# Performance work log

Measured on AMD Instinct MI355X. Metric: run time of the kernel, lower is better.

## Reference

```python
import jax, jax.numpy as jnp
import numpy as np

B, H, T, NCLS = 4096, 300, 43, 80


def setup_inputs() -> dict:
    key = jax.random.key(0)
    ks = jax.random.split(key, 8)
    s = 0.05  # weight init scale
    return {
        "x": jax.random.normal(ks[0], (B, H, T), dtype=jnp.float32),
        "w_ih": jax.random.normal(ks[1], (2, 4 * H, H), dtype=jnp.float32) * s,
        "w_hh": jax.random.normal(ks[2], (2, 4 * H, H), dtype=jnp.float32) * s,
        "b_ih": jax.random.normal(ks[3], (2, 4 * H), dtype=jnp.float32) * s,
        "b_hh": jax.random.normal(ks[4], (2, 4 * H), dtype=jnp.float32) * s,
        "conv_w": jax.random.normal(ks[5], (H,), dtype=jnp.float32) * s,
        "fc_w": jax.random.normal(ks[6], (NCLS, H), dtype=jnp.float32) * s,
        "fc_b": jax.random.normal(ks[7], (NCLS,), dtype=jnp.float32) * s,
    }


def reference(x, w_ih, w_hh, b_ih, b_hh, conv_w, fc_w, fc_b):
    # x: [B, 300, 43]. Each step feeds x[:, :, t] (seq_len=1 LSTM call) to BOTH
    # directions of the 'bidirectional' LSTM, carrying states forward in time.
    # => two independent forward LSTMs (d=0,1) whose hidden states are summed.
    batch = x.shape[0]
    xs = jnp.transpose(x, (2, 0, 1))  # [T, B, H]
    bias = (b_ih + b_hh)[:, None, :]  # [2, 1, 4H]

    def step(carry, xt):
        h, c = carry  # each [2, B, H]
        z = (jnp.einsum('bi,dgi->dbg', xt, w_ih)
             + jnp.einsum('dbh,dgh->dbg', h, w_hh) + bias)  # [2, B, 4H]
        i, f, g, o = jnp.split(z, 4, axis=-1)  # torch gate order i,f,g,o
        c_new = jax.nn.sigmoid(f) * c + jax.nn.sigmoid(i) * jnp.tanh(g)
        h_new = jax.nn.sigmoid(o) * jnp.tanh(c_new)
        return (h_new, c_new), h_new.sum(0)  # sum over the 2 directions

    h0 = jnp.zeros((2, batch, x.shape[1]), dtype=x.dtype)
    _, hsum = jax.lax.scan(step, (h0, h0), xs)  # hsum: [T, B, H]

    hStates = jnp.transpose(hsum, (1, 2, 0))          # [B, H, T]
    M = jnp.tanh(hStates)
    alpha = jnp.einsum('bht,h->bt', M, conv_w)        # conv1d(H->1, k=1), no bias
    alpha = jax.nn.softmax(alpha, axis=-1)            # softmax over time
    r = jnp.einsum('bht,bt->bh', hStates, alpha)      # bmm(hStates, alpha)
    hStar = jnp.tanh(r)                               # [B, H]
    out = hStar @ fc_w.T + fc_b                       # [B, 80]
    return jax.nn.softmax(out, axis=1)
```

## Files before the change

kernel.cpp:

```cpp
#include <hip/hip_runtime.h>
#include <cstdint>
#include <cstddef>

#define B_  4096
#define H_  300
#define T_  43
#define NC_ 80
#define HP  320
#define ND  1280
#define NDD 2560
#define TR  304
#define SB2 (T_ * TR)
#define XZC 4

typedef _Float16 f16;
typedef _Float16 half8 __attribute__((ext_vector_type(8)));
typedef _Float16 half4 __attribute__((ext_vector_type(4)));
typedef float    f32x4 __attribute__((ext_vector_type(4)));

__device__ __forceinline__ void gl_lds16(const void* g, void* l) {
  __builtin_amdgcn_global_load_lds(
      (const __attribute__((address_space(1))) void*)g,
      (__attribute__((address_space(3))) void*)l, 16, 0, 0);
}
__device__ __forceinline__ float sigmoid_(float x) {
  return 1.f / (1.f + __expf(-x));
}
__device__ __forceinline__ float tanh_fast(float x) {
  x = fminf(fmaxf(x, -15.f), 15.f);
  float e = __expf(2.f * x);
  return (e - 1.f) / (e + 1.f);
}

__global__ void prep_weights(const float* __restrict__ w_ih,
                             const float* __restrict__ w_hh,
                             const float* __restrict__ b_ih,
                             const float* __restrict__ b_hh,
                             f16* __restrict__ Wih, f16* __restrict__ Whh,
                             float* __restrict__ bias) {
  int idx = blockIdx.x * 256 + threadIdx.x;
  const int total = NDD * HP;
  if (idx < 2 * total) {
    int which = idx / total;
    int rem = idx % total;
    int row = rem / HP, k = rem % HP;
    int d = row / ND, n = row % ND;
    int jh = n >> 2, g = n & 3;
    float v = 0.f;
    if (jh < H_ && k < H_) {
      const float* W = which ? w_hh : w_ih;
      v = W[((size_t)d * 4 * H_ + g * H_ + jh) * H_ + k];
    }
    (which ? Whh : Wih)[(size_t)row * HP + k] = (f16)v;
  }
  if (idx < NDD) {
    int d = idx / ND, n = idx % ND;
    int jh = n >> 2, g = n & 3;
    float v = 0.f;
    if (jh < H_)
      v = b_ih[d * 4 * H_ + g * H_ + jh] + b_hh[d * 4 * H_ + g * H_ + jh];
    bias[idx] = v;
  }
}

__global__ void prep_xT(const float* __restrict__ x, f16* __restrict__ xT) {
  __shared__ float tile[64][44];
  int b = blockIdx.x, ch = blockIdx.y;
  int h0 = ch * 64;
  for (int idx = threadIdx.x; idx < 64 * T_; idx += 256) {
    int hh = idx / T_, t = idx % T_;
    float v = 0.f;
    if (h0 + hh < H_) v = x[((size_t)b * H_ + h0 + hh) * T_ + t];
    tile[hh][t] = v;
  }
  __syncthreads();
  for (int idx = threadIdx.x; idx < 64 * T_; idx += 256) {
    int t = idx / 64, hh = idx % 64;
    xT[((size_t)t * B_ + b) * HP + h0 + hh] = (f16)tile[hh][t];
  }
}

__global__ void xz_gemm(const f16* __restrict__ Xc,
                        const f16* __restrict__ Wih,
                        half4* __restrict__ xz4) {
  __shared__ f16 As[128 * 32];
  __shared__ f16 Bs[128 * 32];
  const int tid = threadIdx.x;
  const int wave = tid >> 6, lane = tid & 63;
  const int mt = blockIdx.x, nt = blockIdx.y;
  const int lrow4 = lane >> 2, col8 = (lane & 3) << 3;
  const int wm = wave & 1, wn = wave >> 1;
  const int lr = lane & 15, lq = lane >> 4;
  const int kq = lq << 3;

  const f16* Ab = Wih + (size_t)nt * 128 * HP;
  const f16* Bb = Xc + (size_t)mt * 128 * HP;

  f32x4 acc[4][4];
#pragma unroll
  for (int i = 0; i < 4; i++)
#pragma unroll
    for (int j = 0; j < 4; j++) acc[i][j] = (f32x4){0.f, 0.f, 0.f, 0.f};

  for (int kt = 0; kt < HP / 32; ++kt) {
    __syncthreads();
#pragma unroll
    for (int i = 0; i < 2; i++) {
      int r0 = wave * 32 + i * 16;
      gl_lds16(Ab + (size_t)(r0 + lrow4) * HP + kt * 32 + col8, &As[r0 * 32]);
      gl_lds16(Bb + (size_t)(r0 + lrow4) * HP + kt * 32 + col8, &Bs[r0 * 32]);
    }
    __syncthreads();
    half8 af[4], bf[4];
#pragma unroll
    for (int i = 0; i < 4; i++) {
      af[i] = *(const half8*)&As[(wm * 64 + i * 16 + lr) * 32 + kq];
      bf[i] = *(const half8*)&Bs[(wn * 64 + i * 16 + lr) * 32 + kq];
    }
#pragma unroll
    for (int i = 0; i < 4; i++)
#pragma unroll
      for (int j = 0; j < 4; j++)
        acc[i][j] = __builtin_amdgcn_mfma_f32_16x16x32_f16(af[i], bf[j],
                                                           acc[i][j], 0, 0, 0);
  }

  const int dt = nt / 10;
  const int tl = mt >> 5;
#pragma unroll
  for (int i = 0; i < 4; i++) {
    const int jh = (nt % 10) * 32 + wm * 16 + i * 4 + lq;
    if (jh >= H_) continue;
#pragma unroll
    for (int j = 0; j < 4; j++) {
      const int b = (mt & 31) * 128 + wn * 64 + j * 16 + lr;
      half4 o;
#pragma unroll
      for (int r = 0; r < 4; r++) o[r] = (f16)acc[i][j][r];
      xz4[((size_t)(tl * 2 + dt) * HP + jh) * B_ + b] = o;
    }
  }
}

__global__ void lstm_step(const f16* __restrict__ h_prev,
                          f16* __restrict__ h_next,
                          float* __restrict__ c,
                          const f16* __restrict__ Whh,
                          const float* __restrict__ bias,
                          const half4* __restrict__ xz4,
                          f16* __restrict__ hs,
                          int t)
{
  __shared__ __attribute__((aligned(16))) char smem[16384];
  f16* As = (f16*)smem;
  f16* Bs = (f16*)(smem + 8192);
  f16* tile = (f16*)smem;

  const int tid = threadIdx.x;
  const int wave = tid >> 6, lane = tid & 63;
  const int wt = blockIdx.x, bt = blockIdx.y, d = blockIdx.z;
  const int lrow4 = lane >> 2, col8 = (lane & 3) << 3;
  const int wm = wave & 1, wn = wave >> 1;
  const int lr = lane & 15, lq = lane >> 4;
  const int kq = lq << 3;

  const f16* Wb = Whh + ((size_t)d * ND + wt * 128) * HP;
  const f16* hb = h_prev + ((size_t)d * B_ + bt * 128) * HP;

  f32x4 acc[4][4];
#pragma unroll
  for (int i = 0; i < 4; i++)
#pragma unroll
    for (int j = 0; j < 4; j++) acc[i][j] = (f32x4){0.f, 0.f, 0.f, 0.f};

  for (int kt = 0; kt < HP / 32; ++kt) {
    __syncthreads();
#pragma unroll
    for (int i = 0; i < 2; i++) {
      int r0 = wave * 32 + i * 16;
      gl_lds16(Wb + (size_t)(r0 + lrow4) * HP + kt * 32 + col8, &As[r0 * 32]);
      gl_lds16(hb + (size_t)(r0 + lrow4) * HP + kt * 32 + col8, &Bs[r0 * 32]);
    }
    __syncthreads();
    half8 af[4], bf[4];
#pragma unroll
    for (int i = 0; i < 4; i++) {
      af[i] = *(const half8*)&As[(wm * 64 + i * 16 + lr) * 32 + kq];
      bf[i] = *(const half8*)&Bs[(wn * 64 + i * 16 + lr) * 32 + kq];
    }
#pragma unroll
    for (int i = 0; i < 4; i++)
#pragma unroll
      for (int j = 0; j < 4; j++)
        acc[i][j] = __builtin_amdgcn_mfma_f32_16x16x32_f16(af[i], bf[j],
                                                           acc[i][j], 0, 0, 0);
  }

  __syncthreads();

#pragma unroll
  for (int i = 0; i < 4; i++) {
    const int jl = wm * 16 + i * 4 + lq;
    const int jh = wt * 32 + jl;
    float4 b4 = {0.f, 0.f, 0.f, 0.f};
    if (jh < H_) b4 = *(const float4*)&bias[d * ND + 4 * jh];
#pragma unroll
    for (int j = 0; j < 4; j++) {
      const int bl = wn * 64 + j * 16 + lr;
      const int b = bt * 128 + bl;
      f16 hnv = (f16)0.f;
      if (jh < H_) {
        const half4 x4 = xz4[((size_t)d * HP + jh) * B_ + b];
        float zi = acc[i][j][0] + b4.x + (float)x4[0];
        float zf = acc[i][j][1] + b4.y + (float)x4[1];
        float zg = acc[i][j][2] + b4.z + (float)x4[2];
        float zo = acc[i][j][3] + b4.w + (float)x4[3];
        const size_t cidx = ((size_t)d * H_ + jh) * B_ + b;
        float co = c[cidx];
        float cn = sigmoid_(zf) * co + sigmoid_(zi) * tanh_fast(zg);
        float hn = sigmoid_(zo) * tanh_fast(cn);
        c[cidx] = cn;
        hnv = (f16)hn;
      }
      tile[jl * 136 + bl] = hnv;
    }
  }
  __syncthreads();

  {
    const int bl = tid >> 1, jhalf = tid & 1;
    const int b = bt * 128 + bl;
    f16 vals[16];
#pragma unroll
    for (int jj = 0; jj < 16; jj++)
      vals[jj] = tile[(jhalf * 16 + jj) * 136 + bl];
    half8 v0, v1;
#pragma unroll
    for (int r = 0; r < 8; r++) { v0[r] = vals[r]; v1[r] = vals[8 + r]; }

    const int jh0 = wt * 32 + jhalf * 16;
    f16* hdst = h_next + ((size_t)d * B_ + b) * HP + jh0;
    *(half8*)hdst = v0;
    *(half8*)(hdst + 8) = v1;

    if (jh0 < H_) {
      f16* sdst = hs + ((size_t)d * B_ + b) * SB2 + t * TR + jh0;
      *(half8*)sdst = v0;
      *(half8*)(sdst + 8) = v1;
    }
  }
}

__global__ __launch_bounds__(256) void attn1(const f16* __restrict__ hs,
                                             const float* __restrict__ conv_w,
                                             float* __restrict__ alpha_g) {
  __shared__ float cw[TR];
  __shared__ float red[48];
  const int b = blockIdx.x, tid = threadIdx.x;
  const int wave = tid >> 6, lane = tid & 63;
  for (int k = tid; k < TR; k += 256) cw[k] = (k < H_) ? conv_w[k] : 0.f;
  __syncthreads();

  const half4* s0 = (const half4*)(hs + (size_t)b * SB2);
  const half4* s1 = (const half4*)(hs + (size_t)(B_ + b) * SB2);
  for (int t = wave; t < T_; t += 4) {
    const int base = t * (TR / 4);
    float p = 0.f;
    {
      half4 a = s0[base + lane], cc = s1[base + lane];
#pragma unroll
      for (int r = 0; r < 4; r++)
        p += tanh_fast((float)a[r] + (float)cc[r]) * cw[lane * 4 + r];
    }
    if (lane < 12) {
      half4 a = s0[base + 64 + lane], cc = s1[base + 64 + lane];
#pragma unroll
      for (int r = 0; r < 4; r++)
        p += tanh_fast((float)a[r] + (float)cc[r]) * cw[256 + lane * 4 + r];
    }
#pragma unroll
    for (int o = 32; o; o >>= 1) p += __shfl_down(p, o);
    if (lane == 0) red[t] = p;
  }
  __syncthreads();
  if (tid < 64) {
    float a = (tid < T_) ? red[tid] : -1e30f;
    float mx = a;
#pragma unroll
    for (int o = 32; o; o >>= 1) mx = fmaxf(mx, __shfl_xor(mx, o));
    float e = (tid < T_) ? __expf(a - mx) : 0.f;
    float s = e;
#pragma unroll
    for (int o = 32; o; o >>= 1) s += __shfl_xor(s, o);
    if (tid < T_) alpha_g[(size_t)b * 44 + tid] = e / s;
  }
}

__global__ __launch_bounds__(256) void attn2(const f16* __restrict__ hs,
                                             const float* __restrict__ alpha_g,
                                             const float* __restrict__ fc_w,
                                             const float* __restrict__ fc_b,
                                             float* __restrict__ out) {
  __shared__ float al[T_];
  __shared__ float hstar[TR];
  __shared__ float lg[NC_];
  const int b = blockIdx.x, tid = threadIdx.x;
  if (tid < T_) al[tid] = alpha_g[(size_t)b * 44 + tid];
  __syncthreads();

  const f16* s0 = hs + (size_t)b * SB2;
  const f16* s1 = hs + (size_t)(B_ + b) * SB2;
  float r0 = 0.f, r1 = 0.f;
  for (int t = 0; t < T_; t++) {
    const float a = al[t];
    r0 += ((float)s0[t * TR + tid] + (float)s1[t * TR + tid]) * a;
    if (tid < 48)
      r1 += ((float)s0[t * TR + 256 + tid] + (float)s1[t * TR + 256 + tid]) * a;
  }
  hstar[tid] = tanh_fast(r0);
  if (tid < 48) hstar[256 + tid] = tanh_fast(r1);
  __syncthreads();

  const int wave = tid >> 6, lane = tid & 63;
  for (int cls = wave; cls < NC_; cls += 4) {
    float p = 0.f;
    for (int k = lane; k < H_; k += 64) p += hstar[k] * fc_w[(size_t)cls * H_ + k];
#pragma unroll
    for (int o = 32; o; o >>= 1) p += __shfl_down(p, o);
    if (lane == 0) lg[cls] = p + fc_b[cls];
  }
  __syncthreads();
  if (tid < 64) {
    float a0 = (tid < 40) ? lg[tid] : -1e30f;
    float a1 = (tid < 40) ? lg[tid + 40] : -1e30f;
    float mx = fmaxf(a0, a1);
#pragma unroll
    for (int o = 32; o; o >>= 1) mx = fmaxf(mx, __shfl_xor(mx, o));
    float e0 = (tid < 40) ? __expf(a0 - mx) : 0.f;
    float e1 = (tid < 40) ? __expf(a1 - mx) : 0.f;
    float s = e0 + e1;
#pragma unroll
    for (int o = 32; o; o >>= 1) s += __shfl_xor(s, o);
    if (tid < 40) {
      out[(size_t)b * NC_ + tid] = e0 / s;
      out[(size_t)b * NC_ + tid + 40] = e1 / s;
    }
  }
}

extern "C" void kernel_launch(void* const* d_in, const int* in_sizes, int n_in,
                              void* d_out, int out_size, void* d_ws, size_t ws_size,
                              hipStream_t stream) {
  const float* x      = (const float*)d_in[0];
  const float* w_ih   = (const float*)d_in[1];
  const float* w_hh   = (const float*)d_in[2];
  const float* b_ih   = (const float*)d_in[3];
  const float* b_hh   = (const float*)d_in[4];
  const float* conv_w = (const float*)d_in[5];
  const float* fc_w   = (const float*)d_in[6];
  const float* fc_b   = (const float*)d_in[7];
  float* out = (float*)d_out;

  char* p = (char*)d_ws;
  f16* Wih = (f16*)p;   p += (size_t)NDD * HP * sizeof(f16);
  f16* Whh = (f16*)p;   p += (size_t)NDD * HP * sizeof(f16);
  float* bias = (float*)p; p += (size_t)NDD * sizeof(float);
  p = (char*)(((uintptr_t)p + 255) & ~(uintptr_t)255);
  f16* xT = (f16*)p;    p += (size_t)T_ * B_ * HP * sizeof(f16);
  f16* h  = (f16*)p;    p += (size_t)2 * 2 * B_ * HP * sizeof(f16);
  float* c = (float*)p; p += (size_t)2 * B_ * H_ * sizeof(float);
  f16* hs = (f16*)p;    p += (size_t)2 * B_ * SB2 * sizeof(f16);
  half4* xz = (half4*)p; p += (size_t)XZC * 2 * HP * B_ * sizeof(half4);
  float* alpha_g = (float*)p; p += (size_t)B_ * 44 * sizeof(float);

  hipMemsetAsync(h, 0, (size_t)2 * 2 * B_ * HP * sizeof(f16), stream);
  hipMemsetAsync(c, 0, (size_t)2 * B_ * H_ * sizeof(float), stream);

  prep_weights<<<(2 * NDD * HP + 255) / 256, 256, 0, stream>>>(
      w_ih, w_hh, b_ih, b_hh, Wih, Whh, bias);
  prep_xT<<<dim3(B_, 5), 256, 0, stream>>>(x, xT);

  const size_t hstride = (size_t)2 * B_ * HP;
  const size_t xzslab = (size_t)2 * HP * B_;
  int t0 = 0;
  while (t0 < T_) {
    int cn = (T_ - t0 < XZC) ? (T_ - t0) : XZC;
    xz_gemm<<<dim3(cn * 32, 20), 256, 0, stream>>>(
        xT + (size_t)t0 * B_ * HP, Wih, xz);
    for (int tt = 0; tt < cn; ++tt) {
      int t = t0 + tt;
      lstm_step<<<dim3(10, 32, 2), 256, 0, stream>>>(
          h + (size_t)(t & 1) * hstride, h + (size_t)((t + 1) & 1) * hstride,
          c, Whh, bias, xz + (size_t)tt * xzslab, hs, t);
    }
    t0 += cn;
  }

  attn1<<<B_, 256, 0, stream>>>(hs, conv_w, alpha_g);
  attn2<<<B_, 256, 0, stream>>>(hs, alpha_g, fc_w, fc_b, out);
}
```

Before: 2.069 ms.

## Double-buffer LDS tiles in GEMMs and read recurrent h directly from hs

Both xz_gemm and lstm_step now use two LDS buffers, so the next K-slice is loaded while MFMAs run on the current one, with one barrier per iteration instead of two. The h ping-pong buffers are removed: each step reads the previous hidden state straight out of the hs history with a strided layout, and a zeroed buffer stands in for t=0. This drops one global store per step and the extra h buffer. The cost is twice the LDS per block, which can lower occupancy. There is also a risk: the 320-wide K loop now reads past the 304-wide hs slot into the next timestep's slot, which is never initialised. Those values are multiplied by zero-padded weights, but NaN or Inf garbage there could still corrupt the result.

```diff
diff --git a/kernel.cpp b/kernel.cpp
--- a/kernel.cpp
+++ b/kernel.cpp
@@ -83,8 +83,8 @@
 __global__ void xz_gemm(const f16* __restrict__ Xc,
                         const f16* __restrict__ Wih,
                         half4* __restrict__ xz4) {
-  __shared__ f16 As[128 * 32];
-  __shared__ f16 Bs[128 * 32];
+  __shared__ __attribute__((aligned(16))) f16 As[2][4096];
+  __shared__ __attribute__((aligned(16))) f16 Bs[2][4096];
   const int tid = threadIdx.x;
   const int wave = tid >> 6, lane = tid & 63;
   const int mt = blockIdx.x, nt = blockIdx.y;
@@ -102,20 +102,30 @@
 #pragma unroll
     for (int j = 0; j < 4; j++) acc[i][j] = (f32x4){0.f, 0.f, 0.f, 0.f};
 
+#pragma unroll
+  for (int i2 = 0; i2 < 2; i2++) {
+    int r0 = wave * 32 + i2 * 16;
+    gl_lds16(Ab + (size_t)(r0 + lrow4) * HP + col8, &As[0][r0 * 32]);
+    gl_lds16(Bb + (size_t)(r0 + lrow4) * HP + col8, &Bs[0][r0 * 32]);
+  }
+  __syncthreads();
+
   for (int kt = 0; kt < HP / 32; ++kt) {
-    __syncthreads();
-#pragma unroll
-    for (int i = 0; i < 2; i++) {
-      int r0 = wave * 32 + i * 16;
-      gl_lds16(Ab + (size_t)(r0 + lrow4) * HP + kt * 32 + col8, &As[r0 * 32]);
-      gl_lds16(Bb + (size_t)(r0 + lrow4) * HP + kt * 32 + col8, &Bs[r0 * 32]);
-    }
-    __syncthreads();
+    const int cur = kt & 1;
+    if (kt + 1 < HP / 32) {
+      const int nk = (kt + 1) * 32;
+#pragma unroll
+      for (int i2 = 0; i2 < 2; i2++) {
+        int r0 = wave * 32 + i2 * 16;
+        gl_lds16(Ab + (size_t)(r0 + lrow4) * HP + nk + col8, &As[cur ^ 1][r0 * 32]);
+        gl_lds16(Bb + (size_t)(r0 + lrow4) * HP + nk + col8, &Bs[cur ^ 1][r0 * 32]);
+      }
+    }
     half8 af[4], bf[4];
 #pragma unroll
     for (int i = 0; i < 4; i++) {
-      af[i] = *(const half8*)&As[(wm * 64 + i * 16 + lr) * 32 + kq];
-      bf[i] = *(const half8*)&Bs[(wn * 64 + i * 16 + lr) * 32 + kq];
+      af[i] = *(const half8*)&As[cur][(wm * 64 + i * 16 + lr) * 32 + kq];
+      bf[i] = *(const half8*)&Bs[cur][(wn * 64 + i * 16 + lr) * 32 + kq];
     }
 #pragma unroll
     for (int i = 0; i < 4; i++)
@@ -123,6 +133,7 @@
       for (int j = 0; j < 4; j++)
         acc[i][j] = __builtin_amdgcn_mfma_f32_16x16x32_f16(af[i], bf[j],
                                                            acc[i][j], 0, 0, 0);
+    __syncthreads();
   }
 
   const int dt = nt / 10;
@@ -142,8 +153,8 @@
   }
 }
 
-__global__ void lstm_step(const f16* __restrict__ h_prev,
-                          f16* __restrict__ h_next,
+__global__ void lstm_step(const f16* __restrict__ hprev,
+                          long bstride, long dstride,
                           float* __restrict__ c,
                           const f16* __restrict__ Whh,
                           const float* __restrict__ bias,
@@ -151,10 +162,9 @@
                           f16* __restrict__ hs,
                           int t)
 {
-  __shared__ __attribute__((aligned(16))) char smem[16384];
-  f16* As = (f16*)smem;
-  f16* Bs = (f16*)(smem + 8192);
-  f16* tile = (f16*)smem;
+  __shared__ __attribute__((aligned(16))) f16 As[2][4096];
+  __shared__ __attribute__((aligned(16))) f16 Bs[2][4096];
+  f16* tile = &As[0][0];
 
   const int tid = threadIdx.x;
   const int wave = tid >> 6, lane = tid & 63;
@@ -165,7 +175,7 @@
   const int kq = lq << 3;
 
   const f16* Wb = Whh + ((size_t)d * ND + wt * 128) * HP;
-  const f16* hb = h_prev + ((size_t)d * B_ + bt * 128) * HP;
+  const f16* hb = hprev + (size_t)d * dstride + (size_t)(bt * 128) * bstride;
 
   f32x4 acc[4][4];
 #pragma unroll
@@ -173,30 +183,40 @@
 #pragma unroll
     for (int j = 0; j < 4; j++) acc[i][j] = (f32x4){0.f, 0.f, 0.f, 0.f};
 
+#pragma unroll
+  for (int i2 = 0; i2 < 2; i2++) {
+    int r0 = wave * 32 + i2 * 16;
+    gl_lds16(Wb + (size_t)(r0 + lrow4) * HP + col8, &As[0][r0 * 32]);
+    gl_lds16(hb + (size_t)(r0 + lrow4) * bstride + col8, &Bs[0][r0 * 32]);
+  }
+  __syncthreads();
+
   for (int kt = 0; kt < HP / 32; ++kt) {
+    const int cur = kt & 1;
+    if (kt + 1 < HP / 32) {
+      const int nk = (kt + 1) * 32;
+#pragma unroll
+      for (int i2 = 0; i2 < 2; i2++) {
+        int r0 = wave * 32 + i2 * 16;
+        gl_lds16(Wb + (size_t)(r0 + lrow4) * HP + nk + col8, &As[cur ^ 1][r0 * 32]);
+        gl_lds16(hb + (size_t)(r0 + lrow4) * bstride + nk + col8,
+                 &Bs[cur ^ 1][r0 * 32]);
+      }
+    }
+    half8 af[4], bf8[4];
+#pragma unroll
+    for (int i = 0; i < 4; i++) {
+      af[i] = *(const half8*)&As[cur][(wm * 64 + i * 16 + lr) * 32 + kq];
+      bf8[i] = *(const half8*)&Bs[cur][(wn * 64 + i * 16 + lr) * 32 + kq];
+    }
+#pragma unroll
+    for (int i = 0; i < 4; i++)
+#pragma unroll
+      for (int j = 0; j < 4; j++)
+        acc[i][j] = __builtin_amdgcn_mfma_f32_16x16x32_f16(af[i], bf8[j],
+                                                           acc[i][j], 0, 0, 0);
     __syncthreads();
-#pragma unroll
-    for (int i = 0; i < 2; i++) {
-      int r0 = wave * 32 + i * 16;
-      gl_lds16(Wb + (size_t)(r0 + lrow4) * HP + kt * 32 + col8, &As[r0 * 32]);
-      gl_lds16(hb + (size_t)(r0 + lrow4) * HP + kt * 32 + col8, &Bs[r0 * 32]);
-    }
-    __syncthreads();
-    half8 af[4], bf[4];
-#pragma unroll
-    for (int i = 0; i < 4; i++) {
-      af[i] = *(const half8*)&As[(wm * 64 + i * 16 + lr) * 32 + kq];
-      bf[i] = *(const half8*)&Bs[(wn * 64 + i * 16 + lr) * 32 + kq];
-    }
-#pragma unroll
-    for (int i = 0; i < 4; i++)
-#pragma unroll
-      for (int j = 0; j < 4; j++)
-        acc[i][j] = __builtin_amdgcn_mfma_f32_16x16x32_f16(af[i], bf[j],
-                                                           acc[i][j], 0, 0, 0);
-  }
-
-  __syncthreads();
+  }
 
 #pragma unroll
   for (int i = 0; i < 4; i++) {
@@ -230,20 +250,15 @@
   {
     const int bl = tid >> 1, jhalf = tid & 1;
     const int b = bt * 128 + bl;
-    f16 vals[16];
-#pragma unroll
-    for (int jj = 0; jj < 16; jj++)
-      vals[jj] = tile[(jhalf * 16 + jj) * 136 + bl];
-    half8 v0, v1;
-#pragma unroll
-    for (int r = 0; r < 8; r++) { v0[r] = vals[r]; v1[r] = vals[8 + r]; }
-
     const int jh0 = wt * 32 + jhalf * 16;
-    f16* hdst = h_next + ((size_t)d * B_ + b) * HP + jh0;
-    *(half8*)hdst = v0;
-    *(half8*)(hdst + 8) = v1;
-
     if (jh0 < H_) {
+      f16 vals[16];
+#pragma unroll
+      for (int jj = 0; jj < 16; jj++)
+        vals[jj] = tile[(jhalf * 16 + jj) * 136 + bl];
+      half8 v0, v1;
+#pragma unroll
+      for (int r = 0; r < 8; r++) { v0[r] = vals[r]; v1[r] = vals[8 + r]; }
       f16* sdst = hs + ((size_t)d * B_ + b) * SB2 + t * TR + jh0;
       *(half8*)sdst = v0;
       *(half8*)(sdst + 8) = v1;
@@ -367,20 +382,19 @@
   float* bias = (float*)p; p += (size_t)NDD * sizeof(float);
   p = (char*)(((uintptr_t)p + 255) & ~(uintptr_t)255);
   f16* xT = (f16*)p;    p += (size_t)T_ * B_ * HP * sizeof(f16);
-  f16* h  = (f16*)p;    p += (size_t)2 * 2 * B_ * HP * sizeof(f16);
   float* c = (float*)p; p += (size_t)2 * B_ * H_ * sizeof(float);
-  f16* hs = (f16*)p;    p += (size_t)2 * B_ * SB2 * sizeof(f16);
+  f16* zbuf = (f16*)p;  p += ((size_t)2 * B_ * TR + 64) * sizeof(f16);
+  f16* hs = (f16*)p;    p += ((size_t)2 * B_ * SB2 + 64) * sizeof(f16);
   half4* xz = (half4*)p; p += (size_t)XZC * 2 * HP * B_ * sizeof(half4);
   float* alpha_g = (float*)p; p += (size_t)B_ * 44 * sizeof(float);
 
-  hipMemsetAsync(h, 0, (size_t)2 * 2 * B_ * HP * sizeof(f16), stream);
+  hipMemsetAsync(zbuf, 0, ((size_t)2 * B_ * TR + 64) * sizeof(f16), stream);
   hipMemsetAsync(c, 0, (size_t)2 * B_ * H_ * sizeof(float), stream);
 
   prep_weights<<<(2 * NDD * HP + 255) / 256, 256, 0, stream>>>(
       w_ih, w_hh, b_ih, b_hh, Wih, Whh, bias);
   prep_xT<<<dim3(B_, 5), 256, 0, stream>>>(x, xT);
 
-  const size_t hstride = (size_t)2 * B_ * HP;
   const size_t xzslab = (size_t)2 * HP * B_;
   int t0 = 0;
   while (t0 < T_) {
@@ -389,9 +403,11 @@
         xT + (size_t)t0 * B_ * HP, Wih, xz);
     for (int tt = 0; tt < cn; ++tt) {
       int t = t0 + tt;
+      const f16* hp = (t == 0) ? zbuf : (hs + (size_t)(t - 1) * TR);
+      long bs = (t == 0) ? TR : SB2;
+      long ds = (t == 0) ? (long)B_ * TR : (long)B_ * SB2;
       lstm_step<<<dim3(10, 32, 2), 256, 0, stream>>>(
-          h + (size_t)(t & 1) * hstride, h + (size_t)((t + 1) & 1) * hstride,
-          c, Whh, bias, xz + (size_t)tt * xzslab, hs, t);
+          hp, bs, ds, c, Whh, bias, xz + (size_t)tt * xzslab, hs, t);
     }
     t0 += cn;
   }
```

Measured after the change: 2.175 ms. +5.1%, slower.

## Replace per-step LSTM launches with a persistent kernel using group barriers

Applied to the files above, without the earlier changes.

Replaces the chunked input-projection GEMM and 43 per-timestep launches with a single persistent kernel of 640 blocks. Each block loops over time, computes both the x and h projections against a concatenated [Wih|Whh] weight matrix, and synchronises with the 10 blocks sharing its direction and batch tile through an atomic counter barrier. This removes launch overhead and the xz intermediate round trip through memory. The cost is that x·Wih is now computed inside the serial recurrence, h is read with agent-scope atomic loads rather than LDS-staged loads, and correctness depends on all 640 blocks being co-resident so the spin barriers cannot deadlock.

```diff
diff --git a/kernel.cpp b/kernel.cpp
--- a/kernel.cpp
+++ b/kernel.cpp
@@ -7,16 +7,17 @@
 #define T_  43
 #define NC_ 80
 #define HP  320
+#define KT  640
 #define ND  1280
 #define NDD 2560
 #define TR  304
 #define SB2 (T_ * TR)
-#define XZC 4
 
 typedef _Float16 f16;
 typedef _Float16 half8 __attribute__((ext_vector_type(8)));
 typedef _Float16 half4 __attribute__((ext_vector_type(4)));
 typedef float    f32x4 __attribute__((ext_vector_type(4)));
+typedef unsigned long long u64;
 
 __device__ __forceinline__ void gl_lds16(const void* g, void* l) {
   __builtin_amdgcn_global_load_lds(
@@ -31,27 +32,34 @@
   float e = __expf(2.f * x);
   return (e - 1.f) / (e + 1.f);
 }
+__device__ __forceinline__ u64 ld_agent_u64(const u64* p) {
+  return __hip_atomic_load(p, __ATOMIC_RELAXED, __HIP_MEMORY_SCOPE_AGENT);
+}
+__device__ __forceinline__ void st_agent_u64(u64* p, u64 v) {
+  __hip_atomic_store(p, v, __ATOMIC_RELAXED, __HIP_MEMORY_SCOPE_AGENT);
+}
 
 __global__ void prep_weights(const float* __restrict__ w_ih,
                              const float* __restrict__ w_hh,
                              const float* __restrict__ b_ih,
                              const float* __restrict__ b_hh,
-                             f16* __restrict__ Wih, f16* __restrict__ Whh,
-                             float* __restrict__ bias) {
+                             f16* __restrict__ Wc, float* __restrict__ bias) {
   int idx = blockIdx.x * 256 + threadIdx.x;
-  const int total = NDD * HP;
-  if (idx < 2 * total) {
-    int which = idx / total;
-    int rem = idx % total;
-    int row = rem / HP, k = rem % HP;
+  const int total = NDD * KT;
+  if (idx < total) {
+    int row = idx / KT, k = idx % KT;
     int d = row / ND, n = row % ND;
     int jh = n >> 2, g = n & 3;
     float v = 0.f;
-    if (jh < H_ && k < H_) {
-      const float* W = which ? w_hh : w_ih;
-      v = W[((size_t)d * 4 * H_ + g * H_ + jh) * H_ + k];
-    }
-    (which ? Whh : Wih)[(size_t)row * HP + k] = (f16)v;
+    if (jh < H_) {
+      if (k < HP) {
+        if (k < H_) v = w_ih[((size_t)d * 4 * H_ + g * H_ + jh) * H_ + k];
+      } else {
+        int kk = k - HP;
+        if (kk < H_) v = w_hh[((size_t)d * 4 * H_ + g * H_ + jh) * H_ + kk];
+      }
+    }
+    Wc[idx] = (f16)v;
   }
   if (idx < NDD) {
     int d = idx / ND, n = idx % ND;
@@ -80,76 +88,14 @@
   }
 }
 
-__global__ void xz_gemm(const f16* __restrict__ Xc,
-                        const f16* __restrict__ Wih,
-                        half4* __restrict__ xz4) {
-  __shared__ f16 As[128 * 32];
-  __shared__ f16 Bs[128 * 32];
-  const int tid = threadIdx.x;
-  const int wave = tid >> 6, lane = tid & 63;
-  const int mt = blockIdx.x, nt = blockIdx.y;
-  const int lrow4 = lane >> 2, col8 = (lane & 3) << 3;
-  const int wm = wave & 1, wn = wave >> 1;
-  const int lr = lane & 15, lq = lane >> 4;
-  const int kq = lq << 3;
-
-  const f16* Ab = Wih + (size_t)nt * 128 * HP;
-  const f16* Bb = Xc + (size_t)mt * 128 * HP;
-
-  f32x4 acc[4][4];
-#pragma unroll
-  for (int i = 0; i < 4; i++)
-#pragma unroll
-    for (int j = 0; j < 4; j++) acc[i][j] = (f32x4){0.f, 0.f, 0.f, 0.f};
-
-  for (int kt = 0; kt < HP / 32; ++kt) {
-    __syncthreads();
-#pragma unroll
-    for (int i = 0; i < 2; i++) {
-      int r0 = wave * 32 + i * 16;
-      gl_lds16(Ab + (size_t)(r0 + lrow4) * HP + kt * 32 + col8, &As[r0 * 32]);
-      gl_lds16(Bb + (size_t)(r0 + lrow4) * HP + kt * 32 + col8, &Bs[r0 * 32]);
-    }
-    __syncthreads();
-    half8 af[4], bf[4];
-#pragma unroll
-    for (int i = 0; i < 4; i++) {
-      af[i] = *(const half8*)&As[(wm * 64 + i * 16 + lr) * 32 + kq];
-      bf[i] = *(const half8*)&Bs[(wn * 64 + i * 16 + lr) * 32 + kq];
-    }
-#pragma unroll
-    for (int i = 0; i < 4; i++)
-#pragma unroll
-      for (int j = 0; j < 4; j++)
-        acc[i][j] = __builtin_amdgcn_mfma_f32_16x16x32_f16(af[i], bf[j],
-                                                           acc[i][j], 0, 0, 0);
-  }
-
-  const int dt = nt / 10;
-  const int tl = mt >> 5;
-#pragma unroll
-  for (int i = 0; i < 4; i++) {
-    const int jh = (nt % 10) * 32 + wm * 16 + i * 4 + lq;
-    if (jh >= H_) continue;
-#pragma unroll
-    for (int j = 0; j < 4; j++) {
-      const int b = (mt & 31) * 128 + wn * 64 + j * 16 + lr;
-      half4 o;
-#pragma unroll
-      for (int r = 0; r < 4; r++) o[r] = (f16)acc[i][j][r];
-      xz4[((size_t)(tl * 2 + dt) * HP + jh) * B_ + b] = o;
-    }
-  }
-}
-
-__global__ void lstm_step(const f16* __restrict__ h_prev,
-                          f16* __restrict__ h_next,
-                          float* __restrict__ c,
-                          const f16* __restrict__ Whh,
-                          const float* __restrict__ bias,
-                          const half4* __restrict__ xz4,
-                          f16* __restrict__ hs,
-                          int t)
+__global__ __launch_bounds__(256, 3) void lstm_persist(
+    const f16* __restrict__ Wc,
+    const float* __restrict__ bias,
+    const f16* __restrict__ xT,
+    f16* __restrict__ hpp,
+    float* __restrict__ c,
+    f16* __restrict__ hs,
+    unsigned int* __restrict__ bar)
 {
   __shared__ __attribute__((aligned(16))) char smem[16384];
   f16* As = (f16*)smem;
@@ -158,95 +104,145 @@
 
   const int tid = threadIdx.x;
   const int wave = tid >> 6, lane = tid & 63;
-  const int wt = blockIdx.x, bt = blockIdx.y, d = blockIdx.z;
+  const int nt = blockIdx.x;
+  const int bt = blockIdx.y;
+  const int d = nt / 10, wt = nt % 10;
   const int lrow4 = lane >> 2, col8 = (lane & 3) << 3;
   const int wm = wave & 1, wn = wave >> 1;
   const int lr = lane & 15, lq = lane >> 4;
   const int kq = lq << 3;
 
-  const f16* Wb = Whh + ((size_t)d * ND + wt * 128) * HP;
-  const f16* hb = h_prev + ((size_t)d * B_ + bt * 128) * HP;
-
-  f32x4 acc[4][4];
-#pragma unroll
-  for (int i = 0; i < 4; i++)
-#pragma unroll
-    for (int j = 0; j < 4; j++) acc[i][j] = (f32x4){0.f, 0.f, 0.f, 0.f};
-
-  for (int kt = 0; kt < HP / 32; ++kt) {
+  const f16* Wb = Wc + (size_t)nt * 128 * KT;
+  const size_t slab = (size_t)2 * B_ * HP;
+  unsigned int* grpbar = bar + (size_t)(d * 32 + bt) * 64;
+
+  for (int t = 0; t < T_; ++t) {
+    const f16* xrow = xT + ((size_t)t * B_ + bt * 128) * HP;
+    const f16* hread = hpp + (size_t)((t + 1) & 1) * slab + (size_t)d * B_ * HP;
+    f16* hwrite = hpp + (size_t)(t & 1) * slab + (size_t)d * B_ * HP;
+
+    f32x4 acc[4][4];
+#pragma unroll
+    for (int i = 0; i < 4; i++)
+#pragma unroll
+      for (int j = 0; j < 4; j++) acc[i][j] = (f32x4){0.f, 0.f, 0.f, 0.f};
+
+    for (int kt = 0; kt < HP / 32; ++kt) {
+      __syncthreads();
+#pragma unroll
+      for (int i2 = 0; i2 < 2; i2++) {
+        int r0 = wave * 32 + i2 * 16;
+        gl_lds16(Wb + (size_t)(r0 + lrow4) * KT + kt * 32 + col8, &As[r0 * 32]);
+        gl_lds16(xrow + (size_t)(r0 + lrow4) * HP + kt * 32 + col8,
+                 &Bs[r0 * 32]);
+      }
+      __syncthreads();
+      half8 af[4], bf8[4];
+#pragma unroll
+      for (int i = 0; i < 4; i++) {
+        af[i] = *(const half8*)&As[(wm * 64 + i * 16 + lr) * 32 + kq];
+        bf8[i] = *(const half8*)&Bs[(wn * 64 + i * 16 + lr) * 32 + kq];
+      }
+#pragma unroll
+      for (int i = 0; i < 4; i++)
+#pragma unroll
+        for (int j = 0; j < 4; j++)
+          acc[i][j] = __builtin_amdgcn_mfma_f32_16x16x32_f16(af[i], bf8[j],
+                                                             acc[i][j], 0, 0, 0);
+    }
+
+    for (int kt = 0; kt < HP / 32; ++kt) {
+      __syncthreads();
+#pragma unroll
+      for (int i2 = 0; i2 < 2; i2++) {
+        int r0 = wave * 32 + i2 * 16;
+        gl_lds16(Wb + (size_t)(r0 + lrow4) * KT + HP + kt * 32 + col8,
+                 &As[r0 * 32]);
+      }
+      half8 bf8[4];
+#pragma unroll
+      for (int j = 0; j < 4; j++) {
+        const u64* src = (const u64*)(hread +
+            (size_t)(bt * 128 + wn * 64 + j * 16 + lr) * HP + kt * 32 + kq);
+        union { u64 q[2]; half8 h; } u;
+        u.q[0] = ld_agent_u64(src);
+        u.q[1] = ld_agent_u64(src + 1);
+        bf8[j] = u.h;
+      }
+      __syncthreads();
+      half8 af[4];
+#pragma unroll
+      for (int i = 0; i < 4; i++)
+        af[i] = *(const half8*)&As[(wm * 64 + i * 16 + lr) * 32 + kq];
+#pragma unroll
+      for (int i = 0; i < 4; i++)
+#pragma unroll
+        for (int j = 0; j < 4; j++)
+          acc[i][j] = __builtin_amdgcn_mfma_f32_16x16x32_f16(af[i], bf8[j],
+                                                             acc[i][j], 0, 0, 0);
+    }
     __syncthreads();
-#pragma unroll
-    for (int i = 0; i < 2; i++) {
-      int r0 = wave * 32 + i * 16;
-      gl_lds16(Wb + (size_t)(r0 + lrow4) * HP + kt * 32 + col8, &As[r0 * 32]);
-      gl_lds16(hb + (size_t)(r0 + lrow4) * HP + kt * 32 + col8, &Bs[r0 * 32]);
+
+#pragma unroll
+    for (int i = 0; i < 4; i++) {
+      const int jl = wm * 16 + i * 4 + lq;
+      const int jh = wt * 32 + jl;
+      float4 b4 = {0.f, 0.f, 0.f, 0.f};
+      if (jh < H_) b4 = *(const float4*)&bias[d * ND + 4 * jh];
+#pragma unroll
+      for (int j = 0; j < 4; j++) {
+        const int bl = wn * 64 + j * 16 + lr;
+        const int b = bt * 128 + bl;
+        f16 hnv = (f16)0.f;
+        if (jh < H_) {
+          float zi = acc[i][j][0] + b4.x;
+          float zf = acc[i][j][1] + b4.y;
+          float zg = acc[i][j][2] + b4.z;
+          float zo = acc[i][j][3] + b4.w;
+          const size_t cidx = ((size_t)d * H_ + jh) * B_ + b;
+          float co = c[cidx];
+          float cn = sigmoid_(zf) * co + sigmoid_(zi) * tanh_fast(zg);
+          float hn = sigmoid_(zo) * tanh_fast(cn);
+          c[cidx] = cn;
+          hnv = (f16)hn;
+        }
+        tile[jl * 136 + bl] = hnv;
+      }
     }
     __syncthreads();
-    half8 af[4], bf[4];
-#pragma unroll
-    for (int i = 0; i < 4; i++) {
-      af[i] = *(const half8*)&As[(wm * 64 + i * 16 + lr) * 32 + kq];
-      bf[i] = *(const half8*)&Bs[(wn * 64 + i * 16 + lr) * 32 + kq];
-    }
-#pragma unroll
-    for (int i = 0; i < 4; i++)
-#pragma unroll
-      for (int j = 0; j < 4; j++)
-        acc[i][j] = __builtin_amdgcn_mfma_f32_16x16x32_f16(af[i], bf[j],
-                                                           acc[i][j], 0, 0, 0);
-  }
-
-  __syncthreads();
-
-#pragma unroll
-  for (int i = 0; i < 4; i++) {
-    const int jl = wm * 16 + i * 4 + lq;
-    const int jh = wt * 32 + jl;
-    float4 b4 = {0.f, 0.f, 0.f, 0.f};
-    if (jh < H_) b4 = *(const float4*)&bias[d * ND + 4 * jh];
-#pragma unroll
-    for (int j = 0; j < 4; j++) {
-      const int bl = wn * 64 + j * 16 + lr;
+
+    {
+      const int bl = tid >> 1, jhalf = tid & 1;
       const int b = bt * 128 + bl;
-      f16 hnv = (f16)0.f;
-      if (jh < H_) {
-        const half4 x4 = xz4[((size_t)d * HP + jh) * B_ + b];
-        float zi = acc[i][j][0] + b4.x + (float)x4[0];
-        float zf = acc[i][j][1] + b4.y + (float)x4[1];
-        float zg = acc[i][j][2] + b4.z + (float)x4[2];
-        float zo = acc[i][j][3] + b4.w + (float)x4[3];
-        const size_t cidx = ((size_t)d * H_ + jh) * B_ + b;
-        float co = c[cidx];
-        float cn = sigmoid_(zf) * co + sigmoid_(zi) * tanh_fast(zg);
-        float hn = sigmoid_(zo) * tanh_fast(cn);
-        c[cidx] = cn;
-        hnv = (f16)hn;
-      }
-      tile[jl * 136 + bl] = hnv;
-    }
-  }
-  __syncthreads();
-
-  {
-    const int bl = tid >> 1, jhalf = tid & 1;
-    const int b = bt * 128 + bl;
-    f16 vals[16];
-#pragma unroll
-    for (int jj = 0; jj < 16; jj++)
-      vals[jj] = tile[(jhalf * 16 + jj) * 136 + bl];
-    half8 v0, v1;
-#pragma unroll
-    for (int r = 0; r < 8; r++) { v0[r] = vals[r]; v1[r] = vals[8 + r]; }
-
-    const int jh0 = wt * 32 + jhalf * 16;
-    f16* hdst = h_next + ((size_t)d * B_ + b) * HP + jh0;
-    *(half8*)hdst = v0;
-    *(half8*)(hdst + 8) = v1;
-
-    if (jh0 < H_) {
-      f16* sdst = hs + ((size_t)d * B_ + b) * SB2 + t * TR + jh0;
-      *(half8*)sdst = v0;
-      *(half8*)(sdst + 8) = v1;
+      const int jh0 = wt * 32 + jhalf * 16;
+      union { half8 h; u64 q[2]; } v0, v1;
+#pragma unroll
+      for (int jj = 0; jj < 8; jj++) {
+        v0.h[jj] = tile[(jhalf * 16 + jj) * 136 + bl];
+        v1.h[jj] = tile[(jhalf * 16 + 8 + jj) * 136 + bl];
+      }
+      u64* hd = (u64*)(hwrite + (size_t)b * HP + jh0);
+      st_agent_u64(hd + 0, v0.q[0]);
+      st_agent_u64(hd + 1, v0.q[1]);
+      st_agent_u64(hd + 2, v1.q[0]);
+      st_agent_u64(hd + 3, v1.q[1]);
+      if (jh0 < H_) {
+        f16* sdst = hs + ((size_t)d * B_ + b) * SB2 + (size_t)t * TR + jh0;
+        *(half8*)sdst = v0.h;
+        *(half8*)(sdst + 8) = v1.h;
+      }
+    }
+
+    if (t < T_ - 1) {
+      __syncthreads();
+      if (tid == 0) {
+        __hip_atomic_fetch_add(&grpbar[t], 1u, __ATOMIC_RELEASE,
+                               __HIP_MEMORY_SCOPE_AGENT);
+        while (__hip_atomic_load(&grpbar[t], __ATOMIC_RELAXED,
+                                 __HIP_MEMORY_SCOPE_AGENT) < 10u)
+          __builtin_amdgcn_s_sleep(8);
+      }
+      __syncthreads();
     }
   }
 }
@@ -362,39 +358,26 @@
   float* out = (float*)d_out;
 
   char* p = (char*)d_ws;
-  f16* Wih = (f16*)p;   p += (size_t)NDD * HP * sizeof(f16);
-  f16* Whh = (f16*)p;   p += (size_t)NDD * HP * sizeof(f16);
+  f16* Wc = (f16*)p;    p += (size_t)NDD * KT * sizeof(f16);
   float* bias = (float*)p; p += (size_t)NDD * sizeof(float);
   p = (char*)(((uintptr_t)p + 255) & ~(uintptr_t)255);
   f16* xT = (f16*)p;    p += (size_t)T_ * B_ * HP * sizeof(f16);
-  f16* h  = (f16*)p;    p += (size_t)2 * 2 * B_ * HP * sizeof(f16);
   float* c = (float*)p; p += (size_t)2 * B_ * H_ * sizeof(float);
-  f16* hs = (f16*)p;    p += (size_t)2 * B_ * SB2 * sizeof(f16);
-  half4* xz = (half4*)p; p += (size_t)XZC * 2 * HP * B_ * sizeof(half4);
+  f16* hpp = (f16*)p;   p += (size_t)2 * 2 * B_ * HP * sizeof(f16);
+  f16* hs = (f16*)p;    p += ((size_t)2 * B_ * SB2 + 64) * sizeof(f16);
   float* alpha_g = (float*)p; p += (size_t)B_ * 44 * sizeof(float);
-
-  hipMemsetAsync(h, 0, (size_t)2 * 2 * B_ * HP * sizeof(f16), stream);
+  p = (char*)(((uintptr_t)p + 255) & ~(uintptr_t)255);
+  unsigned int* bar = (unsigned int*)p; p += (size_t)64 * 64 * sizeof(unsigned);
+
+  hipMemsetAsync(hpp, 0, (size_t)2 * 2 * B_ * HP * sizeof(f16), stream);
   hipMemsetAsync(c, 0, (size_t)2 * B_ * H_ * sizeof(float), stream);
-
-  prep_weights<<<(2 * NDD * HP + 255) / 256, 256, 0, stream>>>(
-      w_ih, w_hh, b_ih, b_hh, Wih, Whh, bias);
+  hipMemsetAsync(bar, 0, (size_t)64 * 64 * sizeof(unsigned), stream);
+
+  prep_weights<<<(NDD * KT + 255) / 256, 256, 0, stream>>>(
+      w_ih, w_hh, b_ih, b_hh, Wc, bias);
   prep_xT<<<dim3(B_, 5), 256, 0, stream>>>(x, xT);
 
-  const size_t hstride = (size_t)2 * B_ * HP;
-  const size_t xzslab = (size_t)2 * HP * B_;
-  int t0 = 0;
-  while (t0 < T_) {
-    int cn = (T_ - t0 < XZC) ? (T_ - t0) : XZC;
-    xz_gemm<<<dim3(cn * 32, 20), 256, 0, stream>>>(
-        xT + (size_t)t0 * B_ * HP, Wih, xz);
-    for (int tt = 0; tt < cn; ++tt) {
-      int t = t0 + tt;
-      lstm_step<<<dim3(10, 32, 2), 256, 0, stream>>>(
-          h + (size_t)(t & 1) * hstride, h + (size_t)((t + 1) & 1) * hstride,
-          c, Whh, bias, xz + (size_t)tt * xzslab, hs, t);
-    }
-    t0 += cn;
-  }
+  lstm_persist<<<dim3(20, 32), 256, 0, stream>>>(Wc, bias, xT, hpp, c, hs, bar);
 
   attn1<<<B_, 256, 0, stream>>>(hs, conv_w, alpha_g);
   attn2<<<B_, 256, 0, stream>>>(hs, alpha_g, fc_w, fc_b, out);
```

After: 4.313 ms. +108.4%, slower.
